# Performance work log

Hardware: AMD Instinct MI355X
Metric: run time of the kernel (lower is better)

## Reference

```python
import jax, jax.numpy as jnp
import numpy as np

NUM_SAMPLES = 10
MIN_DIST_PTS = 8
TOP_K = 10
GRID_SIZE = 4
GAP = 0.1


def sample_line_points(seg):
    # seg: [N,2,2] (endpoints, ij coords). Vectorized version of the per-group linspace loop.
    lengths = jnp.linalg.norm(seg[:, 0] - seg[:, 1], axis=1)
    n_samp = jnp.clip(jnp.floor(lengths / MIN_DIST_PTS), 2, NUM_SAMPLES)  # [N]
    t = jnp.arange(NUM_SAMPLES, dtype=seg.dtype)  # [S]
    interval = (seg[:, 1] - seg[:, 0]) / (n_samp[:, None] - 1)  # [N,2]
    pts = seg[:, None, 0, :] + t[None, :, None] * interval[:, None, :]  # [N,S,2]
    valid = t[None, :] < n_samp[:, None]  # [N,S]
    pts = jnp.where(valid[..., None], pts, 0.0)  # original zero-pads invalid samples
    return pts, valid


def grid_sample_norm(desc, pts, img_size):
    # desc: [D,Hc,Wc]; pts: [P,2] (i,j) pixel coords in image of size img_size=(H,W).
    # Replicates kornia normalize_pixel_coordinates + F.grid_sample(align_corners=False,
    # bilinear, zero padding), then L2-normalize along D.
    D, Hc, Wc = desc.shape
    H, W = img_size
    gx = 2.0 * pts[:, 1] / (W - 1) - 1.0
    gy = 2.0 * pts[:, 0] / (H - 1) - 1.0
    ix = ((gx + 1.0) * Wc - 1.0) / 2.0
    iy = ((gy + 1.0) * Hc - 1.0) / 2.0
    x0 = jnp.floor(ix)
    y0 = jnp.floor(iy)
    wx1 = ix - x0
    wy1 = iy - y0
    x0i = x0.astype(jnp.int32)
    y0i = y0.astype(jnp.int32)

    def gather(yi, xi):
        inb = (xi >= 0) & (xi < Wc) & (yi >= 0) & (yi < Hc)
        v = desc[:, jnp.clip(yi, 0, Hc - 1), jnp.clip(xi, 0, Wc - 1)]  # [D,P]
        return v * inb

    v = (gather(y0i, x0i) * (1 - wy1) * (1 - wx1)
         + gather(y0i, x0i + 1) * (1 - wy1) * wx1
         + gather(y0i + 1, x0i) * wy1 * (1 - wx1)
         + gather(y0i + 1, x0i + 1) * wy1 * wx1)
    nrm = jnp.linalg.norm(v, axis=0, keepdims=True)
    return v / jnp.maximum(nrm, 1e-12)


def needleman_wunsch(scores):
    # scores: [B,n,m]. Row-wise scan; the within-row dependency
    # v[j+1]=max(v[j], max(prev[j+1], prev[j]+s)) is a prefix-max (cummax).
    b, n, m = scores.shape
    s = scores - GAP
    init = jnp.zeros((b, m + 1), s.dtype)

    def step(prev, row):  # prev [B,m+1], row [B,m]
        a = jnp.maximum(prev[:, 1:], prev[:, :-1] + row)
        new = jnp.maximum(jax.lax.cummax(a, axis=1), 0.0)
        return jnp.concatenate([jnp.zeros((b, 1), s.dtype), new], axis=1), None

    final, _ = jax.lax.scan(step, init, jnp.swapaxes(s, 0, 1))
    return final[:, -1]


def nw_candidate_scores(scores):
    # scores: [N1,N2,S,S] -> (nw [N1,2k], topk [N1,k])
    ls1 = jnp.max(scores, axis=3)
    v1 = ls1 != -1
    ls1 = jnp.where(v1, ls1, 0.0).sum(2) / v1.sum(2)
    ls2 = jnp.max(scores, axis=2)
    v2 = ls2 != -1
    ls2 = jnp.where(v2, ls2, 0.0).sum(2) / v2.sum(2)
    line_scores = (ls1 + ls2) / 2
    topk = jnp.argsort(line_scores, axis=1)[:, -TOP_K:]  # [N1,k]
    top_scores = jnp.take_along_axis(scores, topk[:, :, None, None], axis=1)  # [N1,k,S,S]
    top_scores = jnp.concatenate([top_scores, jnp.flip(top_scores, axis=-1)], axis=1)  # [N1,2k,S,S]
    N1, t2k, n, m = top_scores.shape
    nw = needleman_wunsch(top_scores.reshape(N1 * t2k, n, m)).reshape(N1, t2k)
    return nw, topk


def filter_and_match(scores):
    nw, topk = nw_candidate_scores(scores)
    t2k = nw.shape[1]
    best = jnp.argmax(nw, axis=1) % (t2k // 2)
    return jnp.take_along_axis(topk, best[:, None], axis=1)[:, 0]


def compute_scores(line_seg1, line_seg2, desc1, desc2):
    S = NUM_SAMPLES
    img1 = (desc1.shape[2] * GRID_SIZE, desc1.shape[3] * GRID_SIZE)
    img2 = (desc2.shape[2] * GRID_SIZE, desc2.shape[3] * GRID_SIZE)
    pts1, val1 = sample_line_points(line_seg1)
    pts2, val2 = sample_line_points(line_seg2)
    d1 = grid_sample_norm(desc1[0], pts1.reshape(-1, 2), img1)  # [D, N1*S]
    d2 = grid_sample_norm(desc2[0], pts2.reshape(-1, 2), img2)  # [D, N2*S]
    sc = d1.T @ d2  # [N1*S, N2*S]
    sc = jnp.where(val1.reshape(-1)[:, None], sc, -1.0)
    sc = jnp.where(val2.reshape(-1)[None, :], sc, -1.0)
    N1, N2 = line_seg1.shape[0], line_seg2.shape[0]
    return sc.reshape(N1, S, N2, S).transpose(0, 2, 1, 3)  # [N1,N2,S,S]


def reference(line_seg1, line_seg2, desc1, desc2):
    scores = compute_scores(line_seg1, line_seg2, desc1, desc2)
    matches = filter_and_match(scores)
    # cross check
    matches2 = filter_and_match(scores.transpose(1, 0, 3, 2))
    mutual = matches2[matches] == jnp.arange(line_seg1.shape[0])
    return jnp.where(mutual, matches, -1).astype(jnp.int32)


def setup_inputs() -> dict:
    key = jax.random.key(0)
    k1, k2, k3, k4 = jax.random.split(key, 4)
    IMG = 512.0
    line_seg1 = jax.random.uniform(k1, (512, 2, 2), dtype=jnp.float32) * (IMG - 1.0)
    line_seg2 = jax.random.uniform(k2, (512, 2, 2), dtype=jnp.float32) * (IMG - 1.0)
    desc1 = jax.random.normal(k3, (1, 128, 128, 128), dtype=jnp.float32)
    desc2 = jax.random.normal(k4, (1, 128, 128, 128), dtype=jnp.float32)
    return {"line_seg1": line_seg1, "line_seg2": line_seg2, "desc1": desc1, "desc2": desc2}
```

## Files before the change

### kernel.cpp

```cpp
#include <hip/hip_runtime.h>
#include <cmath>

#define NL 512
#define SS 10
#define DD 128
#define HWC (128 * 128)

typedef _Float16 f16x8 __attribute__((ext_vector_type(8)));
typedef float f32x4 __attribute__((ext_vector_type(4)));

__device__ __forceinline__ void gload_lds16(const void* g, void* l)
{
    __builtin_amdgcn_global_load_lds(
        (__attribute__((address_space(1))) void*)const_cast<void*>(g),
        (__attribute__((address_space(3))) void*)l, 16, 0, 0);
}

__global__ __launch_bounds__(256) void transpose_kernel(
    const float* __restrict__ in1, const float* __restrict__ in2,
    float* __restrict__ out1, float* __restrict__ out2)
{
    const float* in = blockIdx.z ? in2 : in1;
    float* out = blockIdx.z ? out2 : out1;
    __shared__ float tile[32][33];
    int hw0 = blockIdx.x * 32;
    int d0 = blockIdx.y * 32;
    int tx = threadIdx.x, ty = threadIdx.y;
#pragma unroll
    for (int j = 0; j < 32; j += 8)
        tile[ty + j][tx] = in[(size_t)(d0 + ty + j) * HWC + hw0 + tx];
    __syncthreads();
#pragma unroll
    for (int j = 0; j < 32; j += 8)
        out[(size_t)(hw0 + ty + j) * DD + d0 + tx] = tile[tx][ty + j];
}

__device__ __forceinline__ float fetchd(const float* __restrict__ dt, int y, int x, int d)
{
    bool inb = (x >= 0) && (x < 128) && (y >= 0) && (y < 128);
    int yc = y < 0 ? 0 : (y > 127 ? 127 : y);
    int xc = x < 0 ? 0 : (x > 127 ? 127 : x);
    float v = dt[((size_t)(yc * 128 + xc)) * DD + d];
    return inb ? v : 0.0f;
}

__global__ __launch_bounds__(640) void sample_kernel(
    const float* __restrict__ seg1, const float* __restrict__ seg2,
    const float* __restrict__ dt1, const float* __restrict__ dt2,
    float* __restrict__ dd1, float* __restrict__ dd2,
    _Float16* __restrict__ h1, _Float16* __restrict__ m1,
    _Float16* __restrict__ h2, _Float16* __restrict__ m2,
    int* __restrict__ v1, int* __restrict__ v2)
{
#pragma clang fp contract(off)
    int L = blockIdx.x;
    int img = blockIdx.y;
    const float* seg = img ? seg2 : seg1;
    const float* dt = img ? dt2 : dt1;
    float* dd = img ? dd2 : dd1;
    _Float16* ph = img ? h2 : h1;
    _Float16* pm = img ? m2 : m1;
    int* vv = img ? v2 : v1;

    float p0y = seg[L * 4 + 0], p0x = seg[L * 4 + 1];
    float p1y = seg[L * 4 + 2], p1x = seg[L * 4 + 3];
    float dy = p0y - p1y, dx = p0x - p1x;
    float len = sqrtf(dy * dy + dx * dx);
    float nf = floorf(len / 8.0f);
    nf = fminf(fmaxf(nf, 2.0f), 10.0f);
    int ni = (int)nf;
    float ivy = (p1y - p0y) / (nf - 1.0f);
    float ivx = (p1x - p0x) / (nf - 1.0f);

    int t = threadIdx.x >> 6;
    int lane = threadIdx.x & 63;
    int pt = L * SS + t;
    bool val = t < ni;
    int d0 = lane, d1 = lane + 64;
    float o0 = 0.0f, o1 = 0.0f;
    if (val) {
        float py = p0y + (float)t * ivy;
        float px = p0x + (float)t * ivx;
        float gx = 2.0f * px / 511.0f - 1.0f;
        float gy = 2.0f * py / 511.0f - 1.0f;
        float ix = ((gx + 1.0f) * 128.0f - 1.0f) / 2.0f;
        float iy = ((gy + 1.0f) * 128.0f - 1.0f) / 2.0f;
        float x0f = floorf(ix), y0f = floorf(iy);
        float wx = ix - x0f, wy = iy - y0f;
        int x0 = (int)x0f, y0 = (int)y0f;
        float a00 = fetchd(dt, y0, x0, d0),         b00 = fetchd(dt, y0, x0, d1);
        float a01 = fetchd(dt, y0, x0 + 1, d0),     b01 = fetchd(dt, y0, x0 + 1, d1);
        float a10 = fetchd(dt, y0 + 1, x0, d0),     b10 = fetchd(dt, y0 + 1, x0, d1);
        float a11 = fetchd(dt, y0 + 1, x0 + 1, d0), b11 = fetchd(dt, y0 + 1, x0 + 1, d1);
        float omwx = 1.0f - wx, omwy = 1.0f - wy;
        float va = a00 * omwy * omwx + a01 * omwy * wx + a10 * wy * omwx + a11 * wy * wx;
        float vb = b00 * omwy * omwx + b01 * omwy * wx + b10 * wy * omwx + b11 * wy * wx;
        float s = va * va + vb * vb;
#pragma unroll
        for (int m = 1; m < 64; m <<= 1) s += __shfl_xor(s, m);
        float nrm = sqrtf(s);
        float inv = 1.0f;
        o0 = va / fmaxf(nrm, 1e-12f);
        o1 = vb / fmaxf(nrm, 1e-12f);
        (void)inv;
    }
    dd[(size_t)pt * DD + d0] = o0;
    dd[(size_t)pt * DD + d1] = o1;
    float xs0 = o0 * 256.0f;
    _Float16 hh0 = (_Float16)xs0;
    _Float16 mm0 = (_Float16)(xs0 - (float)hh0);
    float xs1 = o1 * 256.0f;
    _Float16 hh1 = (_Float16)xs1;
    _Float16 mm1 = (_Float16)(xs1 - (float)hh1);
    int po0 = ((pt >> 4) << 11) + ((d0 >> 3) << 7) + ((pt & 15) << 3) + (d0 & 7);
    int po1 = ((pt >> 4) << 11) + ((d1 >> 3) << 7) + ((pt & 15) << 3) + (d1 & 7);
    ph[po0] = hh0; pm[po0] = mm0;
    ph[po1] = hh1; pm[po1] = mm1;
    if (lane == 0) vv[pt] = val ? 1 : 0;
}

__device__ __forceinline__ void stage_ks(
    const _Float16* __restrict__ ah, const _Float16* __restrict__ am,
    const _Float16* __restrict__ bh, const _Float16* __restrict__ bm,
    int bi, int bj, int ks, int wave, int lane, char* dst)
{
#pragma unroll
    for (int c = 0; c < 10; ++c) {
        int chunk = wave * 10 + c;
        int side = chunk >= 20;
        int rem = side ? chunk - 20 : chunk;
        int plane = rem >= 10;
        int pb = plane ? rem - 10 : rem;
        const _Float16* base = side ? (plane ? bm : bh) : (plane ? am : ah);
        size_t off = ((size_t)((side ? bj : bi) * 10 + pb) << 11) + (ks << 9) + (lane << 3);
        gload_lds16(base + off, dst + (chunk << 10));
    }
}

__global__ __launch_bounds__(256, 2) void gemm_ls_kernel(
    const _Float16* __restrict__ ah_, const _Float16* __restrict__ am_,
    const _Float16* __restrict__ bh_, const _Float16* __restrict__ bm_,
    const int* __restrict__ v1, const int* __restrict__ v2,
    float* __restrict__ ls, float* __restrict__ lsT)
{
    __shared__ __align__(16) char smem[81920];
    int tid = threadIdx.x;
    int wave = tid >> 6, lane = tid & 63;
    int wr = wave >> 1, wc = wave & 1;

    int flat = blockIdx.y * 32 + blockIdx.x;
    int xcd = flat & 7, n = flat >> 3;
    int bi = (xcd >> 1) * 8 + (n >> 4);
    int bj = (xcd & 1) * 16 + (n & 15);

    int fro = ((lane >> 4) << 8) + ((lane & 15) << 4);

    f32x4 zz = {0.0f, 0.0f, 0.0f, 0.0f};
    f32x4 acc[5][5];
#pragma unroll
    for (int i = 0; i < 5; ++i)
#pragma unroll
        for (int j = 0; j < 5; ++j) acc[i][j] = zz;

    stage_ks(ah_, am_, bh_, bm_, bi, bj, 0, wave, lane, smem);

#pragma unroll 1
    for (int ks = 0; ks < 4; ++ks) {
        char* buf = smem + ((ks & 1) ? 40960 : 0);
        if (ks < 3) {
            stage_ks(ah_, am_, bh_, bm_, bi, bj, ks + 1, wave, lane,
                     smem + (((ks + 1) & 1) ? 40960 : 0));
            asm volatile("s_waitcnt vmcnt(10)" ::: "memory");
        } else {
            asm volatile("s_waitcnt vmcnt(0)" ::: "memory");
        }
        __builtin_amdgcn_sched_barrier(0);
        __builtin_amdgcn_s_barrier();
        __builtin_amdgcn_sched_barrier(0);

        f16x8 B0[5], B1[5];
#pragma unroll
        for (int j = 0; j < 5; ++j) {
            int pb = wc * 5 + j;
            B0[j] = *(const f16x8*)(buf + ((20 + pb) << 10) + fro);
            B1[j] = *(const f16x8*)(buf + ((30 + pb) << 10) + fro);
        }
#pragma unroll
        for (int i = 0; i < 5; ++i) {
            int pb = wr * 5 + i;
            f16x8 fh = *(const f16x8*)(buf + (pb << 10) + fro);
            f16x8 fm = *(const f16x8*)(buf + ((10 + pb) << 10) + fro);
#pragma unroll
            for (int j = 0; j < 5; ++j) {
                f32x4 t = acc[i][j];
                t = __builtin_amdgcn_mfma_f32_16x16x32_f16(fh, B0[j], t, 0, 0, 0);
                t = __builtin_amdgcn_mfma_f32_16x16x32_f16(fh, B1[j], t, 0, 0, 0);
                t = __builtin_amdgcn_mfma_f32_16x16x32_f16(fm, B0[j], t, 0, 0, 0);
                acc[i][j] = t;
            }
        }
        __builtin_amdgcn_sched_barrier(0);
        __builtin_amdgcn_s_barrier();
        __builtin_amdgcn_sched_barrier(0);
    }

    float* scr = (float*)smem;
    const float rescale = 1.0f / 65536.0f;
    for (int half = 0; half < 2; ++half) {
        __syncthreads();
        if (wr == half) {
            float* reg = scr + wc * 6464;
#pragma unroll
            for (int i = 0; i < 5; ++i)
#pragma unroll
                for (int j = 0; j < 5; ++j)
#pragma unroll
                    for (int r = 0; r < 4; ++r) {
                        int row = i * 16 + ((lane >> 4) << 2) + r;
                        int col = j * 16 + (lane & 15);
                        int pi = row / 10, s = row - pi * 10;
                        int pj = col / 10, t = col - pj * 10;
                        reg[(pi * 8 + pj) * 101 + s * 10 + t] = acc[i][j][r] * rescale;
                    }
            asm volatile("s_waitcnt lgkmcnt(0)" ::: "memory");
            const float* mp = reg + lane * 101;
            int iL = bi * 16 + half * 8 + (lane >> 3);
            int jL = bj * 16 + wc * 8 + (lane & 7);
            int va[10], vb[10];
#pragma unroll
            for (int s = 0; s < 10; ++s) va[s] = v1[iL * 10 + s];
#pragma unroll
            for (int t = 0; t < 10; ++t) vb[t] = v2[jL * 10 + t];
            float cmx[10];
#pragma unroll
            for (int t = 0; t < 10; ++t) cmx[t] = -3.0e38f;
            float sum1 = 0.0f; int c1 = 0;
#pragma unroll
            for (int s = 0; s < 10; ++s) {
                float rmx = -3.0e38f;
#pragma unroll
                for (int t = 0; t < 10; ++t) {
                    float v = (va[s] && vb[t]) ? mp[s * 10 + t] : -1.0f;
                    rmx = fmaxf(rmx, v);
                    cmx[t] = fmaxf(cmx[t], v);
                }
                if (rmx != -1.0f) { sum1 += rmx; c1++; }
            }
            float sum2 = 0.0f; int c2 = 0;
#pragma unroll
            for (int t = 0; t < 10; ++t) {
                if (cmx[t] != -1.0f) { sum2 += cmx[t]; c2++; }
            }
            float out = (sum1 / (float)c1 + sum2 / (float)c2) * 0.5f;
            ls[(size_t)iL * NL + jL] = out;
            lsT[(size_t)jL * NL + iL] = out;
        }
    }
}

__global__ __launch_bounds__(64) void topk_kernel(
    const float* __restrict__ ls, const float* __restrict__ lsT, int* __restrict__ topk)
{
    int i = blockIdx.x;
    int dir = blockIdx.y;
    int lane = threadIdx.x;
    const float* src = dir ? &lsT[(size_t)i * NL] : &ls[(size_t)i * NL];

    float v[8];
#pragma unroll
    for (int it = 0; it < 8; ++it) v[it] = src[it * 64 + lane];
    int* outp = &topk[(size_t)(dir * NL + i) * 10];

    for (int p = 9; p >= 0; --p) {
        float bv = -3.0e38f;
        int bi = -1;
#pragma unroll
        for (int it = 0; it < 8; ++it) {
            int j = it * 64 + lane;
            bool better = (v[it] > bv) || (v[it] == bv && j > bi);
            if (better) { bv = v[it]; bi = j; }
        }
#pragma unroll
        for (int m = 1; m < 64; m <<= 1) {
            float ov = __shfl_xor(bv, m);
            int oi = __shfl_xor(bi, m);
            bool better = (ov > bv) || (ov == bv && oi > bi);
            if (better) { bv = ov; bi = oi; }
        }
        if ((bi & 63) == lane) v[bi >> 6] = -3.0e38f;
        if (lane == 0) outp[p] = bi;
    }
}

__global__ __launch_bounds__(256) void nw_kernel(
    const float* __restrict__ d1, const float* __restrict__ d2,
    const int* __restrict__ v1, const int* __restrict__ v2,
    const int* __restrict__ topk, float* __restrict__ nwout)
{
    int L = blockIdx.x;
    int dir = blockIdx.y;
    const float* Ad = dir ? d2 : d1;
    const float* Bd = dir ? d1 : d2;
    const int* vA = dir ? v2 : v1;
    const int* vB = dir ? v1 : v2;
    const int* tk = topk + (size_t)(dir * NL + L) * 10;

    __shared__ float Asl[10 * 132];
    __shared__ float Bsl[10][1320];
    __shared__ float M[10][110];
    __shared__ int vam[10], tks[10];

    int tid = threadIdx.x;
    if (tid < 10) { vam[tid] = vA[L * 10 + tid]; tks[tid] = tk[tid]; }
#pragma unroll
    for (int it = 0; it < 5; ++it) {
        int idx = tid + it * 256;
        int row = idx >> 7, col = idx & 127;
        Asl[row * 132 + col] = Ad[((size_t)L * 10 + row) * DD + col];
    }
    __syncthreads();
#pragma unroll
    for (int it = 0; it < 50; ++it) {
        int idx = tid + it * 256;
        int c = idx / 1280;
        int rem = idx - c * 1280;
        int row = rem >> 7, col = rem & 127;
        Bsl[c][row * 132 + col] = Bd[((size_t)tks[c] * 10 + row) * DD + col];
    }
    __syncthreads();
#pragma unroll
    for (int it = 0; it < 4; ++it) {
        int w = tid + it * 256;
        if (w < 1000) {
            int c = w / 100;
            int rem = w - c * 100;
            int s = rem / 10, t = rem - s * 10;
            const float4* ap = (const float4*)&Asl[s * 132];
            const float4* bp = (const float4*)&Bsl[c][t * 132];
            float acc = 0.0f;
#pragma unroll
            for (int k = 0; k < 32; ++k) {
                float4 a = ap[k], b = bp[k];
                acc = fmaf(a.x, b.x, acc);
                acc = fmaf(a.y, b.y, acc);
                acc = fmaf(a.z, b.z, acc);
                acc = fmaf(a.w, b.w, acc);
            }
            int ok = vam[s] && vB[tks[c] * 10 + t];
            M[c][s * 11 + t] = ok ? acc : -1.0f;
        }
    }
    __syncthreads();

    if (tid < 20) {
        int c = tid % 10, f = tid / 10;
        float prev[11];
#pragma unroll
        for (int p = 0; p < 11; ++p) prev[p] = 0.0f;
#pragma unroll
        for (int s = 0; s < 10; ++s) {
            float oldp = prev[0];
            float run = -3.0e38f;
#pragma unroll
            for (int t = 0; t < 10; ++t) {
                int tt = f ? (9 - t) : t;
                float sc = M[c][s * 11 + tt] - 0.1f;
                float pt1 = prev[t + 1];
                float av = fmaxf(pt1, oldp + sc);
                run = fmaxf(run, av);
                prev[t + 1] = fmaxf(run, 0.0f);
                oldp = pt1;
            }
        }
        nwout[((size_t)(dir * NL + L)) * 20 + f * 10 + c] = prev[10];
    }
}

__global__ __launch_bounds__(512) void final_kernel(
    const float* __restrict__ nw, const int* __restrict__ topk, int* __restrict__ out)
{
    __shared__ int m1[NL], m2[NL];
    int t = threadIdx.x;
    {
        const float* p = nw + (size_t)t * 20;
        float bb = -3.0e38f; int kk = 0;
        for (int k = 0; k < 20; ++k) {
            float v = p[k];
            if (v > bb) { bb = v; kk = k; }
        }
        m1[t] = topk[(size_t)t * 10 + (kk % 10)];
    }
    {
        const float* p = nw + (size_t)(NL + t) * 20;
        float bb = -3.0e38f; int kk = 0;
        for (int k = 0; k < 20; ++k) {
            float v = p[k];
            if (v > bb) { bb = v; kk = k; }
        }
        m2[t] = topk[(size_t)(NL + t) * 10 + (kk % 10)];
    }
    __syncthreads();
    int mt = m1[t];
    out[t] = (m2[mt] == t) ? mt : -1;
}

extern "C" void kernel_launch(void* const* d_in, const int* in_sizes, int n_in,
                              void* d_out, int out_size, void* d_ws, size_t ws_size,
                              hipStream_t stream)
{
    const float* seg1 = (const float*)d_in[0];
    const float* seg2 = (const float*)d_in[1];
    const float* desc1 = (const float*)d_in[2];
    const float* desc2 = (const float*)d_in[3];
    int* out = (int*)d_out;

    char* ws = (char*)d_ws;
    size_t off = 0;
    float* dt1 = (float*)(ws + off); off += (size_t)DD * HWC * 4;
    float* dt2 = (float*)(ws + off); off += (size_t)DD * HWC * 4;
    float* dd1 = (float*)(ws + off); off += (size_t)NL * SS * DD * 4;
    float* dd2 = (float*)(ws + off); off += (size_t)NL * SS * DD * 4;
    int* v1 = (int*)(ws + off); off += (size_t)NL * SS * 4;
    int* v2 = (int*)(ws + off); off += (size_t)NL * SS * 4;
    float* ls = (float*)(ws + off); off += (size_t)NL * NL * 4;
    float* lsT = (float*)(ws + off); off += (size_t)NL * NL * 4;
    int* topk = (int*)(ws + off); off += (size_t)2 * NL * 10 * 4;
    float* nwv = (float*)(ws + off); off += (size_t)2 * NL * 20 * 4;
    size_t PL = (size_t)NL * SS * DD;
    _Float16* h1 = (_Float16*)(ws + off); off += PL * 2;
    _Float16* m1 = (_Float16*)(ws + off); off += PL * 2;
    _Float16* h2 = (_Float16*)(ws + off); off += PL * 2;
    _Float16* m2 = (_Float16*)(ws + off); off += PL * 2;

    transpose_kernel<<<dim3(HWC / 32, DD / 32, 2), dim3(32, 8), 0, stream>>>(
        desc1, desc2, dt1, dt2);
    sample_kernel<<<dim3(NL, 2), 640, 0, stream>>>(
        seg1, seg2, dt1, dt2, dd1, dd2, h1, m1, h2, m2, v1, v2);
    gemm_ls_kernel<<<dim3(32, 32), 256, 0, stream>>>(
        h1, m1, h2, m2, v1, v2, ls, lsT);
    topk_kernel<<<dim3(NL, 2), 64, 0, stream>>>(ls, lsT, topk);
    nw_kernel<<<dim3(NL, 2), 256, 0, stream>>>(dd1, dd2, v1, v2, topk, nwv);
    final_kernel<<<1, 512, 0, stream>>>(nwv, topk, out);
}
```

Measured before the change: 183.7 us.

## Widen GEMM tile to 8 waves and fuse top-k selection into NW kernel

The score GEMM now runs 512-thread blocks, each covering a 160x320 tile. The wider tile doubles B-side columns per block and halves the block count, improving operand reuse. The LDS buffers grow to 120 KB and the per-wave vmcnt waits are rebalanced to match. The separate top-k kernel is removed, and its selection now runs in the first wave of the NW kernel before the B gathers, saving one launch and one round trip through global memory. The trade-offs are higher LDS use per block (limiting occupancy) and a serial top-k step added to the front of each NW block.

Result: no change. 182.2 us (-0.8%).

```diff
diff --git a/kernel.cpp b/kernel.cpp
--- a/kernel.cpp
+++ b/kernel.cpp
@@ -99,10 +99,8 @@
 #pragma unroll
         for (int m = 1; m < 64; m <<= 1) s += __shfl_xor(s, m);
         float nrm = sqrtf(s);
-        float inv = 1.0f;
         o0 = va / fmaxf(nrm, 1e-12f);
         o1 = vb / fmaxf(nrm, 1e-12f);
-        (void)inv;
     }
     dd[(size_t)pt * DD + d0] = o0;
     dd[(size_t)pt * DD + d1] = o1;
@@ -125,33 +123,37 @@
     int bi, int bj, int ks, int wave, int lane, char* dst)
 {
 #pragma unroll
-    for (int c = 0; c < 10; ++c) {
-        int chunk = wave * 10 + c;
-        int side = chunk >= 20;
-        int rem = side ? chunk - 20 : chunk;
-        int plane = rem >= 10;
-        int pb = plane ? rem - 10 : rem;
-        const _Float16* base = side ? (plane ? bm : bh) : (plane ? am : ah);
-        size_t off = ((size_t)((side ? bj : bi) * 10 + pb) << 11) + (ks << 9) + (lane << 3);
-        gload_lds16(base + off, dst + (chunk << 10));
-    }
-}
-
-__global__ __launch_bounds__(256, 2) void gemm_ls_kernel(
+    for (int c = 0; c < 8; ++c) {
+        int chunk = wave + (c << 3);
+        if (chunk < 60) {
+            int side = chunk >= 20;
+            int rem = side ? chunk - 20 : chunk;
+            int nb = side ? 20 : 10;
+            int plane = rem >= nb;
+            int pb = plane ? rem - nb : rem;
+            const _Float16* base = side ? (plane ? bm : bh) : (plane ? am : ah);
+            int gpb = side ? (bj * 20 + pb) : (bi * 10 + pb);
+            size_t off = ((size_t)gpb << 11) + (ks << 9) + (lane << 3);
+            gload_lds16(base + off, dst + (chunk << 10));
+        }
+    }
+}
+
+__global__ __launch_bounds__(512, 2) void gemm_ls_kernel(
     const _Float16* __restrict__ ah_, const _Float16* __restrict__ am_,
     const _Float16* __restrict__ bh_, const _Float16* __restrict__ bm_,
     const int* __restrict__ v1, const int* __restrict__ v2,
     float* __restrict__ ls, float* __restrict__ lsT)
 {
-    __shared__ __align__(16) char smem[81920];
+    __shared__ __align__(16) char smem[122880];
     int tid = threadIdx.x;
     int wave = tid >> 6, lane = tid & 63;
-    int wr = wave >> 1, wc = wave & 1;
-
-    int flat = blockIdx.y * 32 + blockIdx.x;
+    int wr = wave >> 2, wc = wave & 3;
+
+    int flat = blockIdx.x;
     int xcd = flat & 7, n = flat >> 3;
-    int bi = (xcd >> 1) * 8 + (n >> 4);
-    int bj = (xcd & 1) * 16 + (n & 15);
+    int bi = (xcd >> 1) * 8 + (n >> 3);
+    int bj = (xcd & 1) * 8 + (n & 7);
 
     int fro = ((lane >> 4) << 8) + ((lane & 15) << 4);
 
@@ -166,11 +168,12 @@
 
 #pragma unroll 1
     for (int ks = 0; ks < 4; ++ks) {
-        char* buf = smem + ((ks & 1) ? 40960 : 0);
+        char* buf = smem + ((ks & 1) ? 61440 : 0);
         if (ks < 3) {
             stage_ks(ah_, am_, bh_, bm_, bi, bj, ks + 1, wave, lane,
-                     smem + (((ks + 1) & 1) ? 40960 : 0));
-            asm volatile("s_waitcnt vmcnt(10)" ::: "memory");
+                     smem + (((ks + 1) & 1) ? 61440 : 0));
+            if (wave < 4) asm volatile("s_waitcnt vmcnt(8)" ::: "memory");
+            else          asm volatile("s_waitcnt vmcnt(7)" ::: "memory");
         } else {
             asm volatile("s_waitcnt vmcnt(0)" ::: "memory");
         }
@@ -183,7 +186,7 @@
         for (int j = 0; j < 5; ++j) {
             int pb = wc * 5 + j;
             B0[j] = *(const f16x8*)(buf + ((20 + pb) << 10) + fro);
-            B1[j] = *(const f16x8*)(buf + ((30 + pb) << 10) + fro);
+            B1[j] = *(const f16x8*)(buf + ((40 + pb) << 10) + fro);
         }
 #pragma unroll
         for (int i = 0; i < 5; ++i) {
@@ -225,7 +228,7 @@
             asm volatile("s_waitcnt lgkmcnt(0)" ::: "memory");
             const float* mp = reg + lane * 101;
             int iL = bi * 16 + half * 8 + (lane >> 3);
-            int jL = bj * 16 + wc * 8 + (lane & 7);
+            int jL = bj * 32 + wc * 8 + (lane & 7);
             int va[10], vb[10];
 #pragma unroll
             for (int s = 0; s < 10; ++s) va[s] = v1[iL * 10 + s];
@@ -258,44 +261,11 @@
     }
 }
 
-__global__ __launch_bounds__(64) void topk_kernel(
-    const float* __restrict__ ls, const float* __restrict__ lsT, int* __restrict__ topk)
-{
-    int i = blockIdx.x;
-    int dir = blockIdx.y;
-    int lane = threadIdx.x;
-    const float* src = dir ? &lsT[(size_t)i * NL] : &ls[(size_t)i * NL];
-
-    float v[8];
-#pragma unroll
-    for (int it = 0; it < 8; ++it) v[it] = src[it * 64 + lane];
-    int* outp = &topk[(size_t)(dir * NL + i) * 10];
-
-    for (int p = 9; p >= 0; --p) {
-        float bv = -3.0e38f;
-        int bi = -1;
-#pragma unroll
-        for (int it = 0; it < 8; ++it) {
-            int j = it * 64 + lane;
-            bool better = (v[it] > bv) || (v[it] == bv && j > bi);
-            if (better) { bv = v[it]; bi = j; }
-        }
-#pragma unroll
-        for (int m = 1; m < 64; m <<= 1) {
-            float ov = __shfl_xor(bv, m);
-            int oi = __shfl_xor(bi, m);
-            bool better = (ov > bv) || (ov == bv && oi > bi);
-            if (better) { bv = ov; bi = oi; }
-        }
-        if ((bi & 63) == lane) v[bi >> 6] = -3.0e38f;
-        if (lane == 0) outp[p] = bi;
-    }
-}
-
 __global__ __launch_bounds__(256) void nw_kernel(
     const float* __restrict__ d1, const float* __restrict__ d2,
     const int* __restrict__ v1, const int* __restrict__ v2,
-    const int* __restrict__ topk, float* __restrict__ nwout)
+    const float* __restrict__ ls, const float* __restrict__ lsT,
+    int* __restrict__ topkg, float* __restrict__ nwout)
 {
     int L = blockIdx.x;
     int dir = blockIdx.y;
@@ -303,7 +273,7 @@
     const float* Bd = dir ? d1 : d2;
     const int* vA = dir ? v2 : v1;
     const int* vB = dir ? v1 : v2;
-    const int* tk = topk + (size_t)(dir * NL + L) * 10;
+    const float* src = dir ? &lsT[(size_t)L * NL] : &ls[(size_t)L * NL];
 
     __shared__ float Asl[10 * 132];
     __shared__ float Bsl[10][1320];
@@ -311,14 +281,40 @@
     __shared__ int vam[10], tks[10];
 
     int tid = threadIdx.x;
-    if (tid < 10) { vam[tid] = vA[L * 10 + tid]; tks[tid] = tk[tid]; }
+    if (tid < 10) vam[tid] = vA[L * 10 + tid];
 #pragma unroll
     for (int it = 0; it < 5; ++it) {
         int idx = tid + it * 256;
         int row = idx >> 7, col = idx & 127;
         Asl[row * 132 + col] = Ad[((size_t)L * 10 + row) * DD + col];
     }
+    if (tid < 64) {
+        int lane = tid;
+        float v[8];
+#pragma unroll
+        for (int it = 0; it < 8; ++it) v[it] = src[it * 64 + lane];
+        for (int p = 9; p >= 0; --p) {
+            float bv = -3.0e38f;
+            int bi_ = -1;
+#pragma unroll
+            for (int it = 0; it < 8; ++it) {
+                int j = it * 64 + lane;
+                bool better = (v[it] > bv) || (v[it] == bv && j > bi_);
+                if (better) { bv = v[it]; bi_ = j; }
+            }
+#pragma unroll
+            for (int m = 1; m < 64; m <<= 1) {
+                float ov = __shfl_xor(bv, m);
+                int oi = __shfl_xor(bi_, m);
+                bool better = (ov > bv) || (ov == bv && oi > bi_);
+                if (better) { bv = ov; bi_ = oi; }
+            }
+            if ((bi_ & 63) == lane) v[bi_ >> 6] = -3.0e38f;
+            if (lane == 0) tks[p] = bi_;
+        }
+    }
     __syncthreads();
+    if (tid < 10) topkg[(size_t)(dir * NL + L) * 10 + tid] = tks[tid];
 #pragma unroll
     for (int it = 0; it < 50; ++it) {
         int idx = tid + it * 256;
@@ -436,9 +432,9 @@
         desc1, desc2, dt1, dt2);
     sample_kernel<<<dim3(NL, 2), 640, 0, stream>>>(
         seg1, seg2, dt1, dt2, dd1, dd2, h1, m1, h2, m2, v1, v2);
-    gemm_ls_kernel<<<dim3(32, 32), 256, 0, stream>>>(
+    gemm_ls_kernel<<<512, 512, 0, stream>>>(
         h1, m1, h2, m2, v1, v2, ls, lsT);
-    topk_kernel<<<dim3(NL, 2), 64, 0, stream>>>(ls, lsT, topk);
-    nw_kernel<<<dim3(NL, 2), 256, 0, stream>>>(dd1, dd2, v1, v2, topk, nwv);
+    nw_kernel<<<dim3(NL, 2), 256, 0, stream>>>(
+        dd1, dd2, v1, v2, ls, lsT, topk, nwv);
     final_kernel<<<1, 512, 0, stream>>>(nwv, topk, out);
 }
```
